# Kernel tuning notes

Measured on AMD Instinct MI355X. Metric: run time of the kernel, lower is better.

The kernel has to match this reference:

```python
import jax, jax.numpy as jnp
import numpy as np
import math

B, S, D, H = 2, 2048, 1024, 16
DK = D // H


def setup_inputs() -> dict:
    key = jax.random.key(0)
    ks = jax.random.split(key, 12)
    scale = 1.0 / math.sqrt(D)
    inp = {
        'query': jax.random.normal(ks[0], (B, S, D), dtype=jnp.float32),
        'key': jax.random.normal(ks[1], (B, S, D), dtype=jnp.float32),
        'value': jax.random.normal(ks[2], (B, S, D), dtype=jnp.float32),
        'mask': jnp.ones((B, 1, S), dtype=jnp.int32),
        'posr': jax.random.normal(ks[3], (B, S, S), dtype=jnp.float32),
        'Wq': jax.random.normal(ks[4], (D, D), dtype=jnp.float32) * scale,
        'bq': jnp.zeros((D,), dtype=jnp.float32),
        'Wk': jax.random.normal(ks[5], (D, D), dtype=jnp.float32) * scale,
        'bk': jnp.zeros((D,), dtype=jnp.float32),
        'Wv': jax.random.normal(ks[6], (D, D), dtype=jnp.float32) * scale,
        'bv': jnp.zeros((D,), dtype=jnp.float32),
        'Wo': jax.random.normal(ks[7], (D, D), dtype=jnp.float32) * scale,
        'bo': jnp.zeros((D,), dtype=jnp.float32),
    }
    return inp


def _split_heads(x):
    # [B, S, D] -> [B, H, S, DK]
    b, s, _ = x.shape
    return x.reshape(b, s, H, DK).transpose(0, 2, 1, 3)


def reference(query, key, value, mask, posr, Wq, bq, Wk, bk, Wv, bv, Wo, bo):
    q = _split_heads(query @ Wq.T + bq)   # [B,H,S,DK]
    k = _split_heads(key @ Wk.T + bk)
    v = _split_heads(value @ Wv.T + bv)

    scores = jnp.einsum('bhqd,bhkd->bhqk', q, k) / math.sqrt(DK)
    scores = scores + posr[:, None, :, :]            # additive positional bias
    m = mask[:, None, :, :]                           # [B,1,1,S] broadcast
    scores = jnp.where(m == 0, jnp.float32(-1e9), scores)
    p = jax.nn.softmax(scores, axis=-1)
    ctx = jnp.einsum('bhqk,bhkd->bhqd', p, v)        # [B,H,S,DK]
    ctx = ctx.transpose(0, 2, 1, 3).reshape(query.shape[0], -1, D)
    return ctx @ Wo.T + bo
```

## Files before the change

### kernel.cpp

```cpp
#include <hip/hip_runtime.h>
#include <math.h>

#define B_ 2
#define S_ 2048
#define D_ 1024
#define H_ 16
#define DK_ 64

typedef __attribute__((ext_vector_type(8))) short bf16x8;
typedef __attribute__((ext_vector_type(4))) float f32x4;

#define MFMA16(a, b, c) __builtin_amdgcn_mfma_f32_16x16x32_bf16((a), (b), (c), 0, 0, 0)

#define ASYNC16(g, l)                                                          \
    __builtin_amdgcn_global_load_lds(                                          \
        (const __attribute__((address_space(1))) void*)(g),                    \
        (__attribute__((address_space(3))) void*)(l), 16, 0, 0)

#define LOG2E 1.4426950408889634f

__device__ __forceinline__ unsigned short f2bf(float x) {
    unsigned int u = __float_as_uint(x);
    unsigned int r = (u + 0x7fffu + ((u >> 16) & 1u)) >> 16;
    return (unsigned short)r;
}

__global__ __launch_bounds__(256)
void pack_all(const float* __restrict__ q, const float* __restrict__ k,
              const float* __restrict__ v, const float* __restrict__ wq,
              const float* __restrict__ wk, const float* __restrict__ wv,
              const float* __restrict__ wo, unsigned short* __restrict__ ws0)
{
    const int z = blockIdx.z;
    const size_t IN = 4194304, WT = 1048576;
    const float* in;
    unsigned short* dst;
    int n;
    switch (z) {
        case 0: in = q;  dst = ws0;            n = (int)IN; break;
        case 1: in = k;  dst = ws0 + IN;       n = (int)IN; break;
        case 2: in = v;  dst = ws0 + 2*IN;     n = (int)IN; break;
        case 3: in = wq; dst = ws0 + 3*IN;          n = (int)WT; break;
        case 4: in = wk; dst = ws0 + 3*IN + WT;     n = (int)WT; break;
        case 5: in = wv; dst = ws0 + 3*IN + 2*WT;   n = (int)WT; break;
        default:in = wo; dst = ws0 + 3*IN + 3*WT;   n = (int)WT; break;
    }
    const int n4 = n >> 2;
    const int stride = gridDim.x * blockDim.x;
    for (int i = blockIdx.x * blockDim.x + threadIdx.x; i < n4; i += stride) {
        float4 x = ((const float4*)in)[i];
        ushort4 hv;
        hv.x = f2bf(x.x); hv.y = f2bf(x.y); hv.z = f2bf(x.z); hv.w = f2bf(x.w);
        ((ushort4*)dst)[i] = hv;
    }
}

__device__ __forceinline__ void gemm_core2ph(
    const unsigned short* __restrict__ A, const unsigned short* __restrict__ B,
    unsigned short (*As)[128 * 64], unsigned short (*Bs)[64 * 64],
    int m0, int n0, f32x4 (&acc)[4][2])
{
    const int tid  = threadIdx.x;
    const int w    = tid >> 6;
    const int lane = tid & 63;
    const int rA   = lane & 15;
    const int quad = lane >> 4;
    const int wm   = (w & 1) * 64;
    const int wn   = (w >> 1) * 32;

    const int rowc = tid >> 3;
    const int gc   = (tid & 7) ^ (rowc & 7);

#define STA(buf, k0) do {                                                       \
        _Pragma("unroll")                                                       \
        for (int i_ = 0; i_ < 4; ++i_)                                          \
            ASYNC16(A + (size_t)(m0 + i_ * 32 + rowc) * 1024 + (k0) + gc * 8,   \
                    &As[buf][(size_t)(i_ * 256 + w * 64) * 8]);                 \
    } while (0)
#define STB(buf, k0) do {                                                       \
        _Pragma("unroll")                                                       \
        for (int i_ = 0; i_ < 2; ++i_)                                          \
            ASYNC16(B + (size_t)(n0 + i_ * 32 + rowc) * 1024 + (k0) + gc * 8,   \
                    &Bs[buf][(size_t)(i_ * 256 + w * 64) * 8]);                 \
    } while (0)

    STA(0, 0);
    STB(0, 0);
    __syncthreads();

#pragma unroll 1
    for (int k = 0; k < 16; ++k) {
        const int cur = k & 1;
        if (k < 15) {
            STA(cur ^ 1, (k + 1) * 64);
            STB(cur ^ 1, (k + 1) * 64);
        }
#pragma unroll
        for (int ks = 0; ks < 2; ++ks) {
            bf16x8 a[4], bb[2];
#pragma unroll
            for (int mt = 0; mt < 4; ++mt) {
                const int row = wm + mt * 16 + rA;
                a[mt] = *(const bf16x8*)
                    &As[cur][row * 64 + (((ks * 4 + quad) ^ (row & 7)) * 8)];
            }
#pragma unroll
            for (int nt = 0; nt < 2; ++nt) {
                const int row = wn + nt * 16 + rA;
                bb[nt] = *(const bf16x8*)
                    &Bs[cur][row * 64 + (((ks * 4 + quad) ^ (row & 7)) * 8)];
            }
#pragma unroll
            for (int mt = 0; mt < 4; ++mt)
#pragma unroll
                for (int nt = 0; nt < 2; ++nt)
                    acc[mt][nt] = MFMA16(a[mt], bb[nt], acc[mt][nt]);
        }
        __syncthreads();
    }
#undef STA
#undef STB
}

__device__ __forceinline__ void swz512(int& m0, int& n0) {
    const int bid = (int)(blockIdx.x + (blockIdx.y << 4));
    const int swz = (bid & 7) * 64 + (bid >> 3);
    m0 = (swz >> 4) * 128;
    n0 = (swz & 15) * 64;
}

__global__ __launch_bounds__(256, 3)
void gemm_qkv(const unsigned short* __restrict__ ws0,
              const float* __restrict__ bq, const float* __restrict__ bk,
              const float* __restrict__ bv,
              unsigned short* __restrict__ qbuf, unsigned short* __restrict__ kbuf,
              unsigned short* __restrict__ vtbuf)
{
    __shared__ unsigned short As[2][128 * 64];
    __shared__ unsigned short Bs[2][64 * 64];
    const size_t IN = 4194304, WT = 1048576;
    const int z = blockIdx.z;
    const unsigned short* Ap = ws0 + (size_t)z * IN;
    const unsigned short* Bp = ws0 + 3 * IN + (size_t)z * WT;
    const float* bias = (z == 0) ? bq : (z == 1) ? bk : bv;
    unsigned short* dst = (z == 0) ? qbuf : (z == 1) ? kbuf : vtbuf;

    int m0, n0;
    swz512(m0, n0);
    f32x4 acc[4][2] = {};
    gemm_core2ph(Ap, Bp, As, Bs, m0, n0, acc);

    const int tid = threadIdx.x, w = tid >> 6, lane = tid & 63;
    const int quad = lane >> 4, col = lane & 15;
    const int wm = (w & 1) * 64, wn = (w >> 1) * 32;

    if (z == 2) {
        unsigned short* Ts = &As[0][0];
#pragma unroll
        for (int mt = 0; mt < 4; ++mt)
#pragma unroll
            for (int nt = 0; nt < 2; ++nt) {
                const int ln  = wn + nt * 16 + col;
                const int lmb = wm + mt * 16 + quad * 4;
                const float bv_ = bias[n0 + ln];
                ushort4 h;
                h.x = f2bf(acc[mt][nt][0] + bv_);
                h.y = f2bf(acc[mt][nt][1] + bv_);
                h.z = f2bf(acc[mt][nt][2] + bv_);
                h.w = f2bf(acc[mt][nt][3] + bv_);
                *(ushort4*)&Ts[ln * 128 + (lmb ^ ((ln & 7) << 3))] = h;
            }
        __syncthreads();
        const int d    = tid >> 2;
        const int cg   = (tid & 3) * 32;
        const int bb   = m0 >> 11;
        const int sb   = m0 & 2047;
        const int hh   = n0 >> 6;
        unsigned short* drow =
            dst + ((size_t)(bb * 16 + hh) * 64 + d) * 2048 + sb;
#pragma unroll
        for (int j = 0; j < 8; ++j) {
            const int c = cg + j * 4;
            ushort4 hv = *(const ushort4*)&Ts[d * 128 + (c ^ ((d & 7) << 3))];
            *(ushort4*)&drow[c] = hv;
        }
        return;
    }

    const float qscale = (z == 0) ? (0.125f * LOG2E) : 1.0f;
#pragma unroll
    for (int mt = 0; mt < 4; ++mt)
#pragma unroll
        for (int nt = 0; nt < 2; ++nt) {
            f32x4 v = acc[mt][nt];
#pragma unroll
            for (int r = 0; r < 4; ++r) {
                const int m = m0 + wm + mt * 16 + quad * 4 + r;
                const int n = n0 + wn + nt * 16 + col;
                const float val = (v[r] + bias[n]) * qscale;
                const int bb = m >> 11, ss = m & 2047;
                const int hh = n >> 6, dd = n & 63;
                dst[((size_t)(bb * 16 + hh) * 2048 + ss) * 64 + dd] = f2bf(val);
            }
        }
}

__global__ __launch_bounds__(256, 3)
void gemm_out(const unsigned short* __restrict__ Actx,
              const unsigned short* __restrict__ Bwo,
              const float* __restrict__ bias, float* __restrict__ out)
{
    __shared__ unsigned short As[2][128 * 64];
    __shared__ unsigned short Bs[2][64 * 64];
    int m0, n0;
    swz512(m0, n0);
    f32x4 acc[4][2] = {};
    gemm_core2ph(Actx, Bwo, As, Bs, m0, n0, acc);

    const int tid = threadIdx.x, w = tid >> 6, lane = tid & 63;
    const int quad = lane >> 4, col = lane & 15;
    const int wm = (w & 1) * 64, wn = (w >> 1) * 32;
#pragma unroll
    for (int mt = 0; mt < 4; ++mt)
#pragma unroll
        for (int nt = 0; nt < 2; ++nt) {
            f32x4 v = acc[mt][nt];
#pragma unroll
            for (int r = 0; r < 4; ++r) {
                const int m = m0 + wm + mt * 16 + quad * 4 + r;
                const int n = n0 + wn + nt * 16 + col;
                out[(size_t)m * 1024 + n] = v[r] + bias[n];
            }
        }
}

__global__ __launch_bounds__(256, 2)
void attn_mfma(const unsigned short* __restrict__ qbuf,
               const unsigned short* __restrict__ kbuf,
               const unsigned short* __restrict__ vtbuf,
               const float* __restrict__ posr, const int* __restrict__ mask,
               unsigned short* __restrict__ ctxb)
{
    __shared__ unsigned short Ks[3][64 * 64];
    __shared__ unsigned short Vts[3][64 * 64];
    __shared__ unsigned short Ps[128 * 64];

    const int tid  = threadIdx.x;
    const int w    = tid >> 6;
    const int lane = tid & 63;
    const int quad = lane >> 4;
    const int col  = lane & 15;
    const int q0   = blockIdx.x * 128;
    const int h    = blockIdx.y;
    const int b    = blockIdx.z;
    const int wq   = w * 32;

    const size_t headoff = (size_t)(b * 16 + h) * 2048 * 64;
    const unsigned short* Qh  = qbuf + headoff + (size_t)q0 * 64;
    const unsigned short* Kh  = kbuf + headoff;
    const unsigned short* Vth = vtbuf + headoff;

    const int c0 = tid;
    const int c1 = 256 + tid;
    const int r0 = c0 >> 3, g0 = (c0 & 7) ^ (r0 & 7);
    const int r1 = c1 >> 3, g1 = (c1 & 7) ^ (r1 & 7);

#define STAGE(bufidx, kt) do {                                                  \
        ASYNC16(Kh + (size_t)((kt) * 64 + r0) * 64 + g0 * 8,                    \
                &Ks[bufidx][(size_t)(w * 64) * 8]);                             \
        ASYNC16(Kh + (size_t)((kt) * 64 + r1) * 64 + g1 * 8,                    \
                &Ks[bufidx][(size_t)(256 + w * 64) * 8]);                       \
        ASYNC16(Vth + (size_t)r0 * 2048 + (kt) * 64 + g0 * 8,                   \
                &Vts[bufidx][(size_t)(w * 64) * 8]);                            \
        ASYNC16(Vth + (size_t)r1 * 2048 + (kt) * 64 + g1 * 8,                   \
                &Vts[bufidx][(size_t)(256 + w * 64) * 8]);                      \
    } while (0)

    bf16x8 qf[2][2];
#pragma unroll
    for (int mt = 0; mt < 2; ++mt)
#pragma unroll
        for (int ks = 0; ks < 2; ++ks)
            qf[mt][ks] = *(const bf16x8*)
                &Qh[(size_t)(wq + mt * 16 + col) * 64 + ks * 32 + quad * 8];

    const float* prq[2][4];
#pragma unroll
    for (int mt = 0; mt < 2; ++mt)
#pragma unroll
        for (int r = 0; r < 4; ++r)
            prq[mt][r] = posr +
                ((size_t)b * 2048 + (q0 + wq + mt * 16 + quad * 4 + r)) * 2048;
    const int* mrow = mask + (size_t)b * 2048;

    const short one = (short)0x3F80;
    const bf16x8 ones = {one, one, one, one, one, one, one, one};

    STAGE(0, 0);
    STAGE(1, 1);

    float pr[2][4][4];
    int   mk[4];
#pragma unroll
    for (int mt = 0; mt < 2; ++mt)
#pragma unroll
        for (int r = 0; r < 4; ++r)
#pragma unroll
            for (int nt = 0; nt < 4; ++nt)
                pr[mt][r][nt] = prq[mt][r][nt * 16 + col];
#pragma unroll
    for (int nt = 0; nt < 4; ++nt) mk[nt] = mrow[nt * 16 + col];

    f32x4 sc[2][4];
    f32x4 O[2][4] = {};
    f32x4 lacc[2] = {};

    __syncthreads();

#pragma unroll
    for (int mt = 0; mt < 2; ++mt)
#pragma unroll
        for (int nt = 0; nt < 4; ++nt) sc[mt][nt] = (f32x4){0.f, 0.f, 0.f, 0.f};
#pragma unroll
    for (int nt = 0; nt < 4; ++nt)
#pragma unroll
        for (int ks = 0; ks < 2; ++ks) {
            const bf16x8 bk = *(const bf16x8*)
                &Ks[0][(nt * 16 + col) * 64 + (((ks * 4 + quad) ^ (col & 7)) * 8)];
#pragma unroll
            for (int mt = 0; mt < 2; ++mt)
                sc[mt][nt] = MFMA16(qf[mt][ks], bk, sc[mt][nt]);
        }

    int bb = 0, b1 = 1, b2 = 2;
#pragma unroll 1
    for (int t = 0; t < 32; ++t) {
#pragma unroll
        for (int mt = 0; mt < 2; ++mt)
#pragma unroll
            for (int r = 0; r < 4; ++r) {
                const int rowW = wq + mt * 16 + quad * 4 + r;
                const int rsw  = rowW & 7;
#pragma unroll
                for (int nt = 0; nt < 4; ++nt) {
                    const float e = __builtin_amdgcn_exp2f(
                        fmaf(pr[mt][r][nt], LOG2E, sc[mt][nt][r]));
                    unsigned int u = __float_as_uint(e) >> 16;
                    u = mk[nt] ? u : 0u;
                    const int kk = nt * 16 + col;
                    Ps[rowW * 64 + (((kk >> 3) ^ rsw) * 8) + (kk & 7)] =
                        (unsigned short)u;
                }
            }

        __builtin_amdgcn_sched_barrier(0);
        asm volatile("s_waitcnt lgkmcnt(0)" ::: "memory");
        __builtin_amdgcn_s_barrier();
        __builtin_amdgcn_sched_barrier(0);

        if (t < 30) STAGE(b2, t + 2);
        __builtin_amdgcn_sched_barrier(0);

        if (t < 31) {
            const int kn = (t + 1) * 64;
#pragma unroll
            for (int mt = 0; mt < 2; ++mt)
#pragma unroll
                for (int r = 0; r < 4; ++r)
#pragma unroll
                    for (int nt = 0; nt < 4; ++nt)
                        pr[mt][r][nt] = prq[mt][r][kn + nt * 16 + col];
#pragma unroll
            for (int nt = 0; nt < 4; ++nt) mk[nt] = mrow[kn + nt * 16 + col];
        }

#pragma unroll
        for (int ks = 0; ks < 2; ++ks) {
            bf16x8 pa[2];
#pragma unroll
            for (int mt = 0; mt < 2; ++mt)
                pa[mt] = *(const bf16x8*)
                    &Ps[(wq + mt * 16 + col) * 64 + (((ks * 4 + quad) ^ (col & 7)) * 8)];
#pragma unroll
            for (int nt = 0; nt < 4; ++nt) {
                const bf16x8 vb = *(const bf16x8*)
                    &Vts[bb][(nt * 16 + col) * 64 + (((ks * 4 + quad) ^ (col & 7)) * 8)];
#pragma unroll
                for (int mt = 0; mt < 2; ++mt)
                    O[mt][nt] = MFMA16(pa[mt], vb, O[mt][nt]);
            }
#pragma unroll
            for (int mt = 0; mt < 2; ++mt)
                lacc[mt] = MFMA16(pa[mt], ones, lacc[mt]);
        }

        if (t < 31) {
#pragma unroll
            for (int mt = 0; mt < 2; ++mt)
#pragma unroll
                for (int nt = 0; nt < 4; ++nt)
                    sc[mt][nt] = (f32x4){0.f, 0.f, 0.f, 0.f};
#pragma unroll
            for (int nt = 0; nt < 4; ++nt)
#pragma unroll
                for (int ks = 0; ks < 2; ++ks) {
                    const bf16x8 bk = *(const bf16x8*)
                        &Ks[b1][(nt * 16 + col) * 64 + (((ks * 4 + quad) ^ (col & 7)) * 8)];
#pragma unroll
                    for (int mt = 0; mt < 2; ++mt)
                        sc[mt][nt] = MFMA16(qf[mt][ks], bk, sc[mt][nt]);
                }
        }
        const int tmp = bb; bb = b1; b1 = b2; b2 = tmp;
    }

#pragma unroll
    for (int mt = 0; mt < 2; ++mt)
#pragma unroll
        for (int r = 0; r < 4; ++r) {
            const float inv = 1.f / lacc[mt][r];
            const int rowW = wq + mt * 16 + quad * 4 + r;
            const size_t rowoff =
                ((size_t)b * 2048 + (q0 + rowW)) * 1024 + h * 64;
#pragma unroll
            for (int nt = 0; nt < 4; ++nt)
                ctxb[rowoff + nt * 16 + col] = f2bf(O[mt][nt][r] * inv);
        }
#undef STAGE
}

extern "C" void kernel_launch(void* const* d_in, const int* in_sizes, int n_in,
                              void* d_out, int out_size, void* d_ws, size_t ws_size,
                              hipStream_t stream) {
    const float* query = (const float*)d_in[0];
    const float* key   = (const float*)d_in[1];
    const float* value = (const float*)d_in[2];
    const int*   mask  = (const int*)  d_in[3];
    const float* posr  = (const float*)d_in[4];
    const float* Wq    = (const float*)d_in[5];
    const float* bq    = (const float*)d_in[6];
    const float* Wk    = (const float*)d_in[7];
    const float* bk    = (const float*)d_in[8];
    const float* Wv    = (const float*)d_in[9];
    const float* bv    = (const float*)d_in[10];
    const float* Wo    = (const float*)d_in[11];
    const float* bo    = (const float*)d_in[12];
    float* out = (float*)d_out;

    unsigned short* ws0   = (unsigned short*)d_ws;
    const size_t IN = 4194304, WT = 1048576;
    unsigned short* qbuf  = ws0 + 4 * IN;
    unsigned short* kbuf  = ws0 + 5 * IN;
    unsigned short* vtbuf = ws0 + 6 * IN;
    unsigned short* ctxb  = ws0 + 7 * IN;
    const unsigned short* wob = ws0 + 3 * IN + 3 * WT;

    pack_all<<<dim3(512, 1, 7), 256, 0, stream>>>(query, key, value, Wq, Wk, Wv, Wo, ws0);

    gemm_qkv<<<dim3(16, 32, 3), 256, 0, stream>>>(ws0, bq, bk, bv, qbuf, kbuf, vtbuf);

    attn_mfma<<<dim3(16, 16, 2), 256, 0, stream>>>(qbuf, kbuf, vtbuf, posr, mask, ctxb);

    gemm_out<<<dim3(16, 32), 256, 0, stream>>>(ctxb, wob, bo, out);
}
```

Before: 262.0 us.

## Fuse fp32-to-bf16 activation conversion into QKV GEMM A-tile loads

The QKV projection GEMM now reads fp32 query/key/value directly through registers, converts them with packed bf16 conversion instructions and writes them into LDS. The separate pack pass then only converts the weights. This removes a full read and write of the three activation tensors in the pack kernel. In exchange the GEMM re-reads fp32 A tiles (twice the bytes) once per N tile and loses async LDS loads for A, which adds register pressure and conversion work to the GEMM. The packed conversion instruction may also round differently from the software f2bf.

After: 277.5 us. +5.9%, slower.

```diff
diff --git a/kernel.cpp b/kernel.cpp
--- a/kernel.cpp
+++ b/kernel.cpp
@@ -25,27 +25,22 @@
     return (unsigned short)r;
 }
 
+__device__ __forceinline__ unsigned int cvt_pk_bf16(float lo, float hi) {
+    unsigned int r;
+    asm("v_cvt_pk_bf16_f32 %0, %1, %2" : "=v"(r) : "v"(lo), "v"(hi));
+    return r;
+}
+
 __global__ __launch_bounds__(256)
-void pack_all(const float* __restrict__ q, const float* __restrict__ k,
-              const float* __restrict__ v, const float* __restrict__ wq,
-              const float* __restrict__ wk, const float* __restrict__ wv,
-              const float* __restrict__ wo, unsigned short* __restrict__ ws0)
+void pack_all(const float* __restrict__ wq, const float* __restrict__ wk,
+              const float* __restrict__ wv, const float* __restrict__ wo,
+              unsigned short* __restrict__ ws0)
 {
     const int z = blockIdx.z;
     const size_t IN = 4194304, WT = 1048576;
-    const float* in;
-    unsigned short* dst;
-    int n;
-    switch (z) {
-        case 0: in = q;  dst = ws0;            n = (int)IN; break;
-        case 1: in = k;  dst = ws0 + IN;       n = (int)IN; break;
-        case 2: in = v;  dst = ws0 + 2*IN;     n = (int)IN; break;
-        case 3: in = wq; dst = ws0 + 3*IN;          n = (int)WT; break;
-        case 4: in = wk; dst = ws0 + 3*IN + WT;     n = (int)WT; break;
-        case 5: in = wv; dst = ws0 + 3*IN + 2*WT;   n = (int)WT; break;
-        default:in = wo; dst = ws0 + 3*IN + 3*WT;   n = (int)WT; break;
-    }
-    const int n4 = n >> 2;
+    const float* in = (z == 0) ? wq : (z == 1) ? wk : (z == 2) ? wv : wo;
+    unsigned short* dst = ws0 + 3 * IN + (size_t)z * WT;
+    const int n4 = (int)(WT >> 2);
     const int stride = gridDim.x * blockDim.x;
     for (int i = blockIdx.x * blockDim.x + threadIdx.x; i < n4; i += stride) {
         float4 x = ((const float4*)in)[i];
@@ -122,6 +117,92 @@
 #undef STB
 }
 
+__device__ __forceinline__ void gemm_core2ph_f32a(
+    const float* __restrict__ A32, const unsigned short* __restrict__ B,
+    unsigned short (*As)[128 * 64], unsigned short (*Bs)[64 * 64],
+    int m0, int n0, f32x4 (&acc)[4][2])
+{
+    const int tid  = threadIdx.x;
+    const int w    = tid >> 6;
+    const int lane = tid & 63;
+    const int rA   = lane & 15;
+    const int quad = lane >> 4;
+    const int wm   = (w & 1) * 64;
+    const int wn   = (w >> 1) * 32;
+
+    const int rowc = tid >> 3;
+    const int gc   = (tid & 7) ^ (rowc & 7);
+
+    float4 la[8];
+
+#define LDA(k0) do {                                                            \
+        _Pragma("unroll")                                                       \
+        for (int i_ = 0; i_ < 4; ++i_) {                                        \
+            const float* ap_ = A32 +                                            \
+                (size_t)(m0 + i_ * 32 + rowc) * 1024 + (k0) + gc * 8;           \
+            la[i_ * 2]     = *(const float4*)ap_;                               \
+            la[i_ * 2 + 1] = *(const float4*)(ap_ + 4);                         \
+        }                                                                       \
+    } while (0)
+#define WRA(buf) do {                                                           \
+        _Pragma("unroll")                                                       \
+        for (int i_ = 0; i_ < 4; ++i_) {                                        \
+            uint4 w_;                                                           \
+            w_.x = cvt_pk_bf16(la[i_ * 2].x,     la[i_ * 2].y);                 \
+            w_.y = cvt_pk_bf16(la[i_ * 2].z,     la[i_ * 2].w);                 \
+            w_.z = cvt_pk_bf16(la[i_ * 2 + 1].x, la[i_ * 2 + 1].y);             \
+            w_.w = cvt_pk_bf16(la[i_ * 2 + 1].z, la[i_ * 2 + 1].w);             \
+            *(uint4*)&As[buf][(size_t)(i_ * 256 + tid) * 8] = w_;               \
+        }                                                                       \
+    } while (0)
+#define STB(buf, k0) do {                                                       \
+        _Pragma("unroll")                                                       \
+        for (int i_ = 0; i_ < 2; ++i_)                                          \
+            ASYNC16(B + (size_t)(n0 + i_ * 32 + rowc) * 1024 + (k0) + gc * 8,   \
+                    &Bs[buf][(size_t)(i_ * 256 + w * 64) * 8]);                 \
+    } while (0)
+
+    LDA(0);
+    STB(0, 0);
+    WRA(0);
+    __syncthreads();
+
+#pragma unroll 1
+    for (int k = 0; k < 16; ++k) {
+        const int cur = k & 1;
+        if (k < 15) {
+            LDA((k + 1) * 64);
+            STB(cur ^ 1, (k + 1) * 64);
+        }
+#pragma unroll
+        for (int ks = 0; ks < 2; ++ks) {
+            bf16x8 a[4], bb[2];
+#pragma unroll
+            for (int mt = 0; mt < 4; ++mt) {
+                const int row = wm + mt * 16 + rA;
+                a[mt] = *(const bf16x8*)
+                    &As[cur][row * 64 + (((ks * 4 + quad) ^ (row & 7)) * 8)];
+            }
+#pragma unroll
+            for (int nt = 0; nt < 2; ++nt) {
+                const int row = wn + nt * 16 + rA;
+                bb[nt] = *(const bf16x8*)
+                    &Bs[cur][row * 64 + (((ks * 4 + quad) ^ (row & 7)) * 8)];
+            }
+#pragma unroll
+            for (int mt = 0; mt < 4; ++mt)
+#pragma unroll
+                for (int nt = 0; nt < 2; ++nt)
+                    acc[mt][nt] = MFMA16(a[mt], bb[nt], acc[mt][nt]);
+        }
+        if (k < 15) WRA(cur ^ 1);
+        __syncthreads();
+    }
+#undef LDA
+#undef WRA
+#undef STB
+}
+
 __device__ __forceinline__ void swz512(int& m0, int& n0) {
     const int bid = (int)(blockIdx.x + (blockIdx.y << 4));
     const int swz = (bid & 7) * 64 + (bid >> 3);
@@ -130,7 +211,9 @@
 }
 
 __global__ __launch_bounds__(256, 3)
-void gemm_qkv(const unsigned short* __restrict__ ws0,
+void gemm_qkv(const float* __restrict__ query, const float* __restrict__ key,
+              const float* __restrict__ value,
+              const unsigned short* __restrict__ ws0,
               const float* __restrict__ bq, const float* __restrict__ bk,
               const float* __restrict__ bv,
               unsigned short* __restrict__ qbuf, unsigned short* __restrict__ kbuf,
@@ -140,7 +223,7 @@
     __shared__ unsigned short Bs[2][64 * 64];
     const size_t IN = 4194304, WT = 1048576;
     const int z = blockIdx.z;
-    const unsigned short* Ap = ws0 + (size_t)z * IN;
+    const float* Ap = (z == 0) ? query : (z == 1) ? key : value;
     const unsigned short* Bp = ws0 + 3 * IN + (size_t)z * WT;
     const float* bias = (z == 0) ? bq : (z == 1) ? bk : bv;
     unsigned short* dst = (z == 0) ? qbuf : (z == 1) ? kbuf : vtbuf;
@@ -148,7 +231,7 @@
     int m0, n0;
     swz512(m0, n0);
     f32x4 acc[4][2] = {};
-    gemm_core2ph(Ap, Bp, As, Bs, m0, n0, acc);
+    gemm_core2ph_f32a(Ap, Bp, As, Bs, m0, n0, acc);
 
     const int tid = threadIdx.x, w = tid >> 6, lane = tid & 63;
     const int quad = lane >> 4, col = lane & 15;
@@ -455,9 +538,10 @@
     unsigned short* ctxb  = ws0 + 7 * IN;
     const unsigned short* wob = ws0 + 3 * IN + 3 * WT;
 
-    pack_all<<<dim3(512, 1, 7), 256, 0, stream>>>(query, key, value, Wq, Wk, Wv, Wo, ws0);
-
-    gemm_qkv<<<dim3(16, 32, 3), 256, 0, stream>>>(ws0, bq, bk, bv, qbuf, kbuf, vtbuf);
+    pack_all<<<dim3(256, 1, 4), 256, 0, stream>>>(Wq, Wk, Wv, Wo, ws0);
+
+    gemm_qkv<<<dim3(16, 32, 3), 256, 0, stream>>>(query, key, value, ws0,
+                                                  bq, bk, bv, qbuf, kbuf, vtbuf);
 
     attn_mfma<<<dim3(16, 16, 2), 256, 0, stream>>>(qbuf, kbuf, vtbuf, posr, mask, ctxb);
 
```

## Triple-buffer GEMM LDS tiles with explicit vmcnt waits for deeper prefetch

Applied to the files above, without the earlier changes.

Converts the shared GEMM core used by the QKV projection and output projection from double buffering to a three-stage LDS ring. Loads run two k-steps ahead, and the full __syncthreads is replaced by a partial s_waitcnt vmcnt(6) followed by a barrier, so one stage of async global-to-LDS loads can stay in flight during the MFMA work. LDS use grows from 48 KB to 72 KB per block and the launch-bounds occupancy hint drops from 3 to 2, which lowers the number of resident blocks.

Measured after the change: 270.1 us. 1.03x slower.

```diff
diff --git a/kernel.cpp b/kernel.cpp
--- a/kernel.cpp
+++ b/kernel.cpp
@@ -55,7 +55,7 @@
     }
 }
 
-__device__ __forceinline__ void gemm_core2ph(
+__device__ __forceinline__ void gemm_core3ph(
     const unsigned short* __restrict__ A, const unsigned short* __restrict__ B,
     unsigned short (*As)[128 * 64], unsigned short (*Bs)[64 * 64],
     int m0, int n0, f32x4 (&acc)[4][2])
@@ -84,17 +84,23 @@
                     &Bs[buf][(size_t)(i_ * 256 + w * 64) * 8]);                 \
     } while (0)
 
-    STA(0, 0);
-    STB(0, 0);
-    __syncthreads();
+    STA(0, 0);    STB(0, 0);
+    STA(1, 64);   STB(1, 64);
+    __builtin_amdgcn_sched_barrier(0);
+    asm volatile("s_waitcnt vmcnt(6)" ::: "memory");
+    __builtin_amdgcn_s_barrier();
+    __builtin_amdgcn_sched_barrier(0);
 
 #pragma unroll 1
     for (int k = 0; k < 16; ++k) {
-        const int cur = k & 1;
-        if (k < 15) {
-            STA(cur ^ 1, (k + 1) * 64);
-            STB(cur ^ 1, (k + 1) * 64);
-        }
+        const int cur = k % 3;
+        if (k < 14) {
+            const int nb = (k + 2) % 3;
+            STA(nb, (k + 2) * 64);
+            STB(nb, (k + 2) * 64);
+        }
+        __builtin_amdgcn_sched_barrier(0);
+
 #pragma unroll
         for (int ks = 0; ks < 2; ++ks) {
             bf16x8 a[4], bb[2];
@@ -116,7 +122,14 @@
                 for (int nt = 0; nt < 2; ++nt)
                     acc[mt][nt] = MFMA16(a[mt], bb[nt], acc[mt][nt]);
         }
-        __syncthreads();
+
+        __builtin_amdgcn_sched_barrier(0);
+        if (k < 14)
+            asm volatile("s_waitcnt vmcnt(6) lgkmcnt(0)" ::: "memory");
+        else
+            asm volatile("s_waitcnt vmcnt(0) lgkmcnt(0)" ::: "memory");
+        __builtin_amdgcn_s_barrier();
+        __builtin_amdgcn_sched_barrier(0);
     }
 #undef STA
 #undef STB
@@ -129,15 +142,15 @@
     n0 = (swz & 15) * 64;
 }
 
-__global__ __launch_bounds__(256, 3)
+__global__ __launch_bounds__(256, 2)
 void gemm_qkv(const unsigned short* __restrict__ ws0,
               const float* __restrict__ bq, const float* __restrict__ bk,
               const float* __restrict__ bv,
               unsigned short* __restrict__ qbuf, unsigned short* __restrict__ kbuf,
               unsigned short* __restrict__ vtbuf)
 {
-    __shared__ unsigned short As[2][128 * 64];
-    __shared__ unsigned short Bs[2][64 * 64];
+    __shared__ unsigned short As[3][128 * 64];
+    __shared__ unsigned short Bs[3][64 * 64];
     const size_t IN = 4194304, WT = 1048576;
     const int z = blockIdx.z;
     const unsigned short* Ap = ws0 + (size_t)z * IN;
@@ -148,7 +161,7 @@
     int m0, n0;
     swz512(m0, n0);
     f32x4 acc[4][2] = {};
-    gemm_core2ph(Ap, Bp, As, Bs, m0, n0, acc);
+    gemm_core3ph(Ap, Bp, As, Bs, m0, n0, acc);
 
     const int tid = threadIdx.x, w = tid >> 6, lane = tid & 63;
     const int quad = lane >> 4, col = lane & 15;
@@ -205,17 +218,17 @@
         }
 }
 
-__global__ __launch_bounds__(256, 3)
+__global__ __launch_bounds__(256, 2)
 void gemm_out(const unsigned short* __restrict__ Actx,
               const unsigned short* __restrict__ Bwo,
               const float* __restrict__ bias, float* __restrict__ out)
 {
-    __shared__ unsigned short As[2][128 * 64];
-    __shared__ unsigned short Bs[2][64 * 64];
+    __shared__ unsigned short As[3][128 * 64];
+    __shared__ unsigned short Bs[3][64 * 64];
     int m0, n0;
     swz512(m0, n0);
     f32x4 acc[4][2] = {};
-    gemm_core2ph(Actx, Bwo, As, Bs, m0, n0, acc);
+    gemm_core3ph(Actx, Bwo, As, Bs, m0, n0, acc);
 
     const int tid = threadIdx.x, w = tid >> 6, lane = tid & 63;
     const int quad = lane >> 4, col = lane & 15;
```
